# Optimization experiments

Measured on AMD Instinct MI355X. Metric: run time of the kernel, lower is better.

Reference implementation:

```python
import jax, jax.numpy as jnp
import numpy as np

B, S, I = 16, 512, 64
D, H, L, F = 512, 8, 6, 2048
MAX_REL = 32
EPS = 1e-5


def setup_inputs() -> dict:
    key = jax.random.key(0)
    ks = jax.random.split(key, 16)
    sc = 0.02
    inp = {
        "x": jax.random.normal(ks[0], (B, S, I), dtype=jnp.float32),
        "in_W": jax.random.normal(ks[1], (I, D), dtype=jnp.float32) * sc,
        "in_b": jnp.zeros((D,), jnp.float32),
        "rel_emb": jax.random.normal(ks[2], (2 * MAX_REL + 1, D), dtype=jnp.float32) * sc,
        "qkvo_W": jax.random.normal(ks[3], (L, 4, D, D), dtype=jnp.float32) * sc,
        "qkvo_b": jnp.zeros((L, 4, D), jnp.float32),
        "ln_g": jnp.ones((L, 2, D), jnp.float32),
        "ln_b": jnp.zeros((L, 2, D), jnp.float32),
        "ff_W1": jax.random.normal(ks[4], (L, D, F), dtype=jnp.float32) * sc,
        "ff_b1": jnp.zeros((L, F), jnp.float32),
        "ff_W2": jax.random.normal(ks[5], (L, F, D), dtype=jnp.float32) * sc,
        "ff_b2": jnp.zeros((L, D), jnp.float32),
        "out_W": jax.random.normal(ks[6], (D, 1), dtype=jnp.float32) * sc,
        "out_b": jnp.zeros((1,), jnp.float32),
    }
    return inp


def _layernorm(x, g, b):
    mu = jnp.mean(x, axis=-1, keepdims=True)
    var = jnp.mean((x - mu) ** 2, axis=-1, keepdims=True)
    return (x - mu) * jax.lax.rsqrt(var + EPS) * g + b


def reference(x, in_W, in_b, rel_emb, qkvo_W, qkvo_b, ln_g, ln_b, ff_W1, ff_b1, ff_W2, ff_b2, out_W, out_b):
    b, s, _ = x.shape
    dk = D // H
    h = x @ in_W + in_b  # (B,S,D)
    # relative positional encoding: mean over query axis of gathered embeddings
    pos = jnp.arange(s)
    rel = jnp.clip(pos[:, None] - pos[None, :], -MAX_REL, MAX_REL) + MAX_REL  # (S,S)
    rp = rel_emb[rel]  # (S,S,D)
    h = h + rp.mean(axis=0)[None]  # broadcast over batch

    def layer(h, p):
        Wqkvo, bqkvo, g, bl, W1, b1, W2, b2 = p
        def proj(i):
            return (h @ Wqkvo[i] + bqkvo[i]).reshape(b, s, H, dk).transpose(0, 2, 1, 3)
        q, k, v = proj(0), proj(1), proj(2)  # (B,H,S,dk)
        scores = jnp.einsum("bhqd,bhkd->bhqk", q, k) / jnp.sqrt(jnp.float32(dk))
        attn = jax.nn.softmax(scores, axis=-1)
        ctx = jnp.einsum("bhqk,bhkd->bhqd", attn, v)
        ctx = ctx.transpose(0, 2, 1, 3).reshape(b, s, D)
        ao = ctx @ Wqkvo[3] + bqkvo[3]
        h1 = _layernorm(h + ao, g[0], bl[0])
        ff = jax.nn.relu(h1 @ W1 + b1) @ W2 + b2
        h2 = _layernorm(h1 + ff, g[1], bl[1])
        return h2, None

    h, _ = jax.lax.scan(layer, h, (qkvo_W, qkvo_b, ln_g, ln_b, ff_W1, ff_b1, ff_W2, ff_b2))
    out = h @ out_W + out_b  # (B,S,1)
    return out
```

## Files before the change

### kernel.cpp

```cpp
#include <hip/hip_runtime.h>
#include <math.h>

#define B 16
#define S 512
#define IN 64
#define D 512
#define H 8
#define DK 64
#define L 6
#define F 2048
#define BS (B*S)
#define EPS 1e-5f

typedef short short8 __attribute__((ext_vector_type(8)));
typedef short short4v __attribute__((ext_vector_type(4)));
typedef float floatx4 __attribute__((ext_vector_type(4)));

static __device__ inline short f2bf(float x) {
    unsigned u = __float_as_uint(x);
    unsigned r = (u + 0x7fffu + ((u >> 16) & 1u)) >> 16;
    return (short)r;
}
static __device__ inline float bf2f(short s) {
    return __uint_as_float(((unsigned)(unsigned short)s) << 16);
}

__global__ __launch_bounds__(256) void pe_kernel(const float* __restrict__ rel_emb,
                                                 float* __restrict__ pe) {
    int k = blockIdx.x;
    int d = threadIdx.x;
    float acc0 = 0.f, acc1 = 0.f;
    for (int r = 0; r < 65; ++r) {
        float w;
        if (r == 0)       w = (float)max(0, k - 31);
        else if (r == 64) w = (float)max(0, S - (k + 32));
        else {
            int qpos = k + r - 32;
            w = (qpos >= 0 && qpos < S) ? 1.f : 0.f;
        }
        acc0 += w * rel_emb[r * D + d];
        acc1 += w * rel_emb[r * D + d + 256];
    }
    pe[k * D + d]       = acc0 * (1.f / (float)S);
    pe[k * D + d + 256] = acc1 * (1.f / (float)S);
}

__global__ __launch_bounds__(256) void wtrans_kernel(const float* __restrict__ src,
                                                     short* __restrict__ dst,
                                                     int K, int N) {
    __shared__ float Ls[32][33];
    const int z = blockIdx.z, kb = blockIdx.y, nb = blockIdx.x;
    const int tx = threadIdx.x & 31, ty = threadIdx.x >> 5;
    src += (size_t)z * K * N;
    dst += (size_t)z * K * N;
#pragma unroll
    for (int i = 0; i < 4; ++i)
        Ls[ty + i * 8][tx] = src[(size_t)(kb * 32 + ty + i * 8) * N + nb * 32 + tx];
    __syncthreads();
#pragma unroll
    for (int i = 0; i < 4; ++i) {
        int n = nb * 32 + ty + i * 8;
        dst[(size_t)n * K + kb * 32 + tx] = f2bf(Ls[tx][ty + i * 8]);
    }
}

__global__ __launch_bounds__(256) void cvt_kernel(const float* __restrict__ in,
                                                  short* __restrict__ out) {
    int i = (blockIdx.x * 256 + threadIdx.x) * 4;
    float4 v = *(const float4*)(in + i);
    short4v o;
    o.x = f2bf(v.x); o.y = f2bf(v.y); o.z = f2bf(v.z); o.w = f2bf(v.w);
    *(short4v*)(out + i) = o;
}

__global__ __launch_bounds__(256) void vtrans_kernel(const short* __restrict__ v,
                                                     short* __restrict__ vt) {
    __shared__ short Ls[64 * 72];
    const int bh = blockIdx.y, jt = blockIdx.x * 64;
    const int t = threadIdx.x;
    const int r = t >> 2, cg = t & 3;
    *(short8*)&Ls[r * 72 + cg * 8] =
        *(const short8*)(v + ((size_t)bh * S + jt + r) * DK + cg * 8);
    *(short8*)&Ls[r * 72 + 32 + cg * 8] =
        *(const short8*)(v + ((size_t)bh * S + jt + r) * DK + 32 + cg * 8);
    __syncthreads();
    const int d = t >> 2, sg = t & 3;
    short tmp[16];
#pragma unroll
    for (int i = 0; i < 16; ++i) tmp[i] = Ls[(sg * 16 + i) * 72 + d];
    short* dst = vt + ((size_t)bh * DK + d) * S + jt + sg * 16;
    *(short8*)(dst)     = *(short8*)&tmp[0];
    *(short8*)(dst + 8) = *(short8*)&tmp[8];
}

#define GLL(SRC, DST) __builtin_amdgcn_global_load_lds( \
    (const __attribute__((address_space(1))) void*)(SRC), \
    (__attribute__((address_space(3))) void*)(DST), 16, 0, 0)

__global__ __launch_bounds__(256) void mfma_gemm(
    const short* __restrict__ A, const short* __restrict__ Bt,
    const float* __restrict__ bias, short* __restrict__ Cb,
    int M, int N, int K, int mode,
    const float* __restrict__ pe, long wz, long bz, long cz)
{
    __shared__ short As[2][128 * 32];
    __shared__ short Bs[2][128 * 32];

    const int z = blockIdx.z;
    const short* Bz = Bt + (size_t)z * wz;
    const float* bb = bias + (size_t)z * bz;

    const int t = threadIdx.x;
    const int w = t >> 6, lane = t & 63;
    const int wm = w >> 1, wn = w & 1;
    const int ln15 = lane & 15, lq = lane >> 4;
    const int bm = blockIdx.y, bn = blockIdx.x;

    const int ml = lane >> 2;
    const int kb = ((lane & 3) - (ml >> 1)) & 3;
    const short* Ag0 = A  + (size_t)(bm * 128 + w * 16 + ml)       * K + kb * 8;
    const short* Ag1 = A  + (size_t)(bm * 128 + (w + 4) * 16 + ml) * K + kb * 8;
    const short* Bg0 = Bz + (size_t)(bn * 128 + w * 16 + ml)       * K + kb * 8;
    const short* Bg1 = Bz + (size_t)(bn * 128 + (w + 4) * 16 + ml) * K + kb * 8;
    const int so0 = w * 512, so1 = (w + 4) * 512;

    floatx4 acc[4][4] = {};
    const int slot = ln15 * 4 + ((lq + (ln15 >> 1)) & 3);

    GLL(Ag0, &As[0][so0]);
    GLL(Ag1, &As[0][so1]);
    GLL(Bg0, &Bs[0][so0]);
    GLL(Bg1, &Bs[0][so1]);

    int buf = 0;
    for (int kt = 0; kt < K; kt += 32) {
        __syncthreads();
        const int ktn = kt + 32;
        if (ktn < K) {
            GLL(Ag0 + ktn, &As[buf ^ 1][so0]);
            GLL(Ag1 + ktn, &As[buf ^ 1][so1]);
            GLL(Bg0 + ktn, &Bs[buf ^ 1][so0]);
            GLL(Bg1 + ktn, &Bs[buf ^ 1][so1]);
        }
        short8 af[4], bf[4];
#pragma unroll
        for (int mt = 0; mt < 4; ++mt) {
            af[mt] = *(const short8*)&As[buf][((wm * 4 + mt) * 64 + slot) * 8];
            bf[mt] = *(const short8*)&Bs[buf][((wn * 4 + mt) * 64 + slot) * 8];
        }
#pragma unroll
        for (int mt = 0; mt < 4; ++mt)
#pragma unroll
            for (int nt = 0; nt < 4; ++nt)
                acc[mt][nt] = __builtin_amdgcn_mfma_f32_16x16x32_bf16(
                    af[mt], bf[nt], acc[mt][nt], 0, 0, 0);
        buf ^= 1;
    }

    short* Cbz = Cb + (size_t)z * cz;
#pragma unroll
    for (int mt = 0; mt < 4; ++mt) {
#pragma unroll
        for (int nt = 0; nt < 4; ++nt) {
            const int col = bn * 128 + wn * 64 + nt * 16 + ln15;
            const int row0 = bm * 128 + wm * 64 + mt * 16 + lq * 4;
            const float bc = bb[col];
#pragma unroll
            for (int reg = 0; reg < 4; ++reg) {
                const int r = row0 + reg;
                float v = acc[mt][nt][reg] + bc;
                if (mode == 1) v = fmaxf(v, 0.f);
                else if (mode == 2) v += pe[(size_t)(r & (S - 1)) * D + col];
                if (mode == 3) {
                    const int bi = r >> 9, si = r & (S - 1);
                    const int hh = col >> 6, dd = col & 63;
                    Cbz[(((size_t)(bi * H + hh) * S + si) * DK + dd)] = f2bf(v);
                } else {
                    Cb[(size_t)r * N + col] = f2bf(v);
                }
            }
        }
    }
}

__global__ __launch_bounds__(256) void attn_mfma(
    const short* __restrict__ qg, const short* __restrict__ kg,
    const short* __restrict__ vtg, short* __restrict__ ctx)
{
    __shared__ short Ks[64 * 72];
    __shared__ short Vs[64 * 72];
    __shared__ short Ps[4][16 * 72];

    const int t = threadIdx.x;
    const int w = t >> 6, lane = t & 63;
    const int ln15 = lane & 15, lq = lane >> 4;
    const int bh = blockIdx.y, bi = bh >> 3, hh = bh & 7;
    const int qbase = blockIdx.x * 64 + w * 16;

    short8 qf0, qf1;
    {
        const short* qrow = qg + ((size_t)bh * S + qbase + ln15) * DK;
        qf0 = *(const short8*)(qrow + lq * 8);
        qf1 = *(const short8*)(qrow + 32 + lq * 8);
    }
    floatx4 o[4] = {};
    float mrow[4] = {-1e30f, -1e30f, -1e30f, -1e30f};
    float lrow[4] = {};

    const int sr = t >> 2, scg = t & 3;
    const short* kbase = kg  + (size_t)bh * S * DK;
    const short* vtb   = vtg + (size_t)bh * DK * S;

    for (int jt = 0; jt < S; jt += 64) {
        __syncthreads();
        *(short8*)&Ks[sr * 72 + scg * 8] =
            *(const short8*)(kbase + (size_t)(jt + sr) * DK + scg * 8);
        *(short8*)&Ks[sr * 72 + 32 + scg * 8] =
            *(const short8*)(kbase + (size_t)(jt + sr) * DK + 32 + scg * 8);
        *(short8*)&Vs[sr * 72 + scg * 8] =
            *(const short8*)(vtb + (size_t)sr * S + jt + scg * 8);
        *(short8*)&Vs[sr * 72 + 32 + scg * 8] =
            *(const short8*)(vtb + (size_t)sr * S + jt + 32 + scg * 8);
        __syncthreads();

        floatx4 sc[4];
#pragma unroll
        for (int nt = 0; nt < 4; ++nt) {
            floatx4 s4 = {};
            short8 kf0 = *(const short8*)&Ks[(nt * 16 + ln15) * 72 + lq * 8];
            short8 kf1 = *(const short8*)&Ks[(nt * 16 + ln15) * 72 + 32 + lq * 8];
            s4 = __builtin_amdgcn_mfma_f32_16x16x32_bf16(qf0, kf0, s4, 0, 0, 0);
            s4 = __builtin_amdgcn_mfma_f32_16x16x32_bf16(qf1, kf1, s4, 0, 0, 0);
#pragma unroll
            for (int r = 0; r < 4; ++r) s4[r] *= 0.125f;
            sc[nt] = s4;
        }

        float rmax[4];
#pragma unroll
        for (int r = 0; r < 4; ++r)
            rmax[r] = fmaxf(fmaxf(sc[0][r], sc[1][r]), fmaxf(sc[2][r], sc[3][r]));
#pragma unroll
        for (int off = 1; off < 16; off <<= 1)
#pragma unroll
            for (int r = 0; r < 4; ++r)
                rmax[r] = fmaxf(rmax[r], __shfl_xor(rmax[r], off));

        float mnew[4], alpha[4], psum[4];
#pragma unroll
        for (int r = 0; r < 4; ++r) {
            mnew[r]  = fmaxf(mrow[r], rmax[r]);
            alpha[r] = __expf(mrow[r] - mnew[r]);
            psum[r]  = 0.f;
        }
#pragma unroll
        for (int nt = 0; nt < 4; ++nt)
#pragma unroll
            for (int r = 0; r < 4; ++r) {
                float p = __expf(sc[nt][r] - mnew[r]);
                psum[r] += p;
                Ps[w][(lq * 4 + r) * 72 + nt * 16 + ln15] = f2bf(p);
            }
#pragma unroll
        for (int off = 1; off < 16; off <<= 1)
#pragma unroll
            for (int r = 0; r < 4; ++r)
                psum[r] += __shfl_xor(psum[r], off);
#pragma unroll
        for (int r = 0; r < 4; ++r) {
            lrow[r] = lrow[r] * alpha[r] + psum[r];
            mrow[r] = mnew[r];
        }
#pragma unroll
        for (int dv = 0; dv < 4; ++dv)
#pragma unroll
            for (int r = 0; r < 4; ++r)
                o[dv][r] *= alpha[r];

        short8 pf0 = *(const short8*)&Ps[w][ln15 * 72 + lq * 8];
        short8 pf1 = *(const short8*)&Ps[w][ln15 * 72 + 32 + lq * 8];
#pragma unroll
        for (int dv = 0; dv < 4; ++dv) {
            short8 vf0 = *(const short8*)&Vs[(dv * 16 + ln15) * 72 + lq * 8];
            short8 vf1 = *(const short8*)&Vs[(dv * 16 + ln15) * 72 + 32 + lq * 8];
            o[dv] = __builtin_amdgcn_mfma_f32_16x16x32_bf16(pf0, vf0, o[dv], 0, 0, 0);
            o[dv] = __builtin_amdgcn_mfma_f32_16x16x32_bf16(pf1, vf1, o[dv], 0, 0, 0);
        }
    }

    float inv[4];
#pragma unroll
    for (int r = 0; r < 4; ++r) inv[r] = 1.f / lrow[r];
#pragma unroll
    for (int dv = 0; dv < 4; ++dv)
#pragma unroll
        for (int r = 0; r < 4; ++r) {
            const int s = qbase + lq * 4 + r;
            const int col = hh * DK + dv * 16 + ln15;
            ctx[((size_t)bi * S + s) * D + col] = f2bf(o[dv][r] * inv[r]);
        }
}

__global__ __launch_bounds__(128) void ln_kernel(
    const short* __restrict__ a, const short* __restrict__ bres,
    const float* __restrict__ g, const float* __restrict__ beta,
    short* __restrict__ outb)
{
    const int row = blockIdx.x;
    const int t = threadIdx.x;
    const short4v xa = *(const short4v*)(a    + (size_t)row * D + t * 4);
    const short4v xb = *(const short4v*)(bres + (size_t)row * D + t * 4);
    float x0 = bf2f(xa.x) + bf2f(xb.x), x1 = bf2f(xa.y) + bf2f(xb.y);
    float x2 = bf2f(xa.z) + bf2f(xb.z), x3 = bf2f(xa.w) + bf2f(xb.w);
    float s  = x0 + x1 + x2 + x3;
    float s2 = x0 * x0 + x1 * x1 + x2 * x2 + x3 * x3;
#pragma unroll
    for (int o = 32; o > 0; o >>= 1) {
        s  += __shfl_down(s, o);
        s2 += __shfl_down(s2, o);
    }
    __shared__ float red[2][2];
    const int wave = t >> 6;
    if ((t & 63) == 0) { red[wave][0] = s; red[wave][1] = s2; }
    __syncthreads();
    s  = red[0][0] + red[1][0];
    s2 = red[0][1] + red[1][1];
    const float mu  = s * (1.f / (float)D);
    const float var = s2 * (1.f / (float)D) - mu * mu;
    const float r   = rsqrtf(var + EPS);
    const float4 gg = *(const float4*)(g    + t * 4);
    const float4 bb = *(const float4*)(beta + t * 4);
    short4v ob;
    ob.x = f2bf((x0 - mu) * r * gg.x + bb.x);
    ob.y = f2bf((x1 - mu) * r * gg.y + bb.y);
    ob.z = f2bf((x2 - mu) * r * gg.z + bb.z);
    ob.w = f2bf((x3 - mu) * r * gg.w + bb.w);
    *(short4v*)(outb + (size_t)row * D + t * 4) = ob;
}

__global__ __launch_bounds__(256) void out_kernel(
    const short* __restrict__ h, const float* __restrict__ ow,
    const float* __restrict__ ob, float* __restrict__ out)
{
    const int wave = threadIdx.x >> 6;
    const int lane = threadIdx.x & 63;
    const int row  = blockIdx.x * 4 + wave;
    const short* hp = h + (size_t)row * D;
    float s = 0.f;
#pragma unroll
    for (int u = 0; u < 8; ++u) {
        int d = lane + u * 64;
        s += bf2f(hp[d]) * ow[d];
    }
#pragma unroll
    for (int o = 32; o > 0; o >>= 1) s += __shfl_down(s, o);
    if (lane == 0) out[row] = s + ob[0];
}

extern "C" void kernel_launch(void* const* d_in, const int* in_sizes, int n_in,
                              void* d_out, int out_size, void* d_ws, size_t ws_size,
                              hipStream_t stream) {
    const float* x       = (const float*)d_in[0];
    const float* in_W    = (const float*)d_in[1];
    const float* in_b    = (const float*)d_in[2];
    const float* rel_emb = (const float*)d_in[3];
    const float* qkvo_W  = (const float*)d_in[4];
    const float* qkvo_b  = (const float*)d_in[5];
    const float* ln_g    = (const float*)d_in[6];
    const float* ln_bb   = (const float*)d_in[7];
    const float* ff_W1   = (const float*)d_in[8];
    const float* ff_b1   = (const float*)d_in[9];
    const float* ff_W2   = (const float*)d_in[10];
    const float* ff_b2   = (const float*)d_in[11];
    const float* out_W   = (const float*)d_in[12];
    const float* out_b   = (const float*)d_in[13];
    float* out = (float*)d_out;

    const size_t HSZ = (size_t)BS * D;
    float* pe     = (float*)d_ws;
    short* h_bf   = (short*)(pe + (size_t)S * D);
    short* h1_bf  = h_bf  + HSZ;
    short* tmp_bf = h1_bf + HSZ;
    short* qkv_bf = tmp_bf + HSZ;
    short* xb     = qkv_bf + 4 * HSZ;
    short* wt_qkvo = xb + (size_t)BS * IN;
    short* wt_ff1  = wt_qkvo + (size_t)L * 4 * D * D;
    short* wt_ff2  = wt_ff1  + (size_t)L * D * F;
    short* wt_in   = wt_ff2  + (size_t)L * F * D;

    const size_t CZ = (size_t)B * H * S * DK;
    short* qb = qkv_bf;
    short* kb = qkv_bf + CZ;
    short* vb = qkv_bf + 2 * CZ;
    short* vt = qkv_bf + 3 * CZ;
    short* ctx_bf = vb;
    short* ff1_bf = qkv_bf;

    dim3 blk(256);

    pe_kernel<<<dim3(S), blk, 0, stream>>>(rel_emb, pe);
    cvt_kernel<<<dim3(BS * IN / 1024), blk, 0, stream>>>(x, xb);
    wtrans_kernel<<<dim3(D / 32, IN / 32, 1), blk, 0, stream>>>(in_W, wt_in, IN, D);
    wtrans_kernel<<<dim3(D / 32, D / 32, 4 * L), blk, 0, stream>>>(qkvo_W, wt_qkvo, D, D);
    wtrans_kernel<<<dim3(F / 32, D / 32, L), blk, 0, stream>>>(ff_W1, wt_ff1, D, F);
    wtrans_kernel<<<dim3(D / 32, F / 32, L), blk, 0, stream>>>(ff_W2, wt_ff2, F, D);

    mfma_gemm<<<dim3(D / 128, BS / 128, 1), blk, 0, stream>>>(
        xb, wt_in, in_b, h_bf, BS, D, IN, 2, pe, 0, 0, 0);

    for (int l = 0; l < L; ++l) {
        const float* bl = qkvo_b + (size_t)l * 4 * D;
        mfma_gemm<<<dim3(D / 128, BS / 128, 3), blk, 0, stream>>>(
            h_bf, wt_qkvo + (size_t)l * 4 * D * D, bl, qkv_bf, BS, D, D, 3,
            nullptr, (long)D * D, (long)D, (long)CZ);
        vtrans_kernel<<<dim3(S / 64, B * H), blk, 0, stream>>>(vb, vt);
        attn_mfma<<<dim3(S / 64, B * H), blk, 0, stream>>>(qb, kb, vt, ctx_bf);
        mfma_gemm<<<dim3(D / 128, BS / 128, 1), blk, 0, stream>>>(
            ctx_bf, wt_qkvo + (size_t)(l * 4 + 3) * D * D, bl + 3 * D, tmp_bf,
            BS, D, D, 0, nullptr, 0, 0, 0);
        ln_kernel<<<dim3(BS), dim3(128), 0, stream>>>(
            h_bf, tmp_bf, ln_g + (size_t)l * 2 * D, ln_bb + (size_t)l * 2 * D, h1_bf);
        mfma_gemm<<<dim3(F / 128, BS / 128, 1), blk, 0, stream>>>(
            h1_bf, wt_ff1 + (size_t)l * D * F, ff_b1 + (size_t)l * F, ff1_bf,
            BS, F, D, 1, nullptr, 0, 0, 0);
        mfma_gemm<<<dim3(D / 128, BS / 128, 1), blk, 0, stream>>>(
            ff1_bf, wt_ff2 + (size_t)l * F * D, ff_b2 + (size_t)l * D, tmp_bf,
            BS, D, F, 0, nullptr, 0, 0, 0);
        ln_kernel<<<dim3(BS), dim3(128), 0, stream>>>(
            h1_bf, tmp_bf, ln_g + (size_t)l * 2 * D + D, ln_bb + (size_t)l * 2 * D + D,
            h_bf);
    }

    out_kernel<<<dim3(BS / 4), blk, 0, stream>>>(h_bf, out_W, out_b, out);
}
```

Measured before the change: 1.271 ms.

## Split-K the Wo and FF2 GEMMs and reduce partials inside layernorm

The output-projection and second FFN GEMMs now split K in two via blockIdx.z, writing fp32 partial results to two buffers. The residual layernorm kernel sums both partials, the bias and the residual before normalising. This doubles the block count for these N=512 GEMMs so more compute units are busy. In exchange it adds fp32 partial traffic to and from memory, and the workspace layout changes.

```diff
diff --git a/kernel.cpp b/kernel.cpp
--- a/kernel.cpp
+++ b/kernel.cpp
@@ -100,15 +100,15 @@
 __global__ __launch_bounds__(256) void mfma_gemm(
     const short* __restrict__ A, const short* __restrict__ Bt,
     const float* __restrict__ bias, short* __restrict__ Cb,
-    int M, int N, int K, int mode,
-    const float* __restrict__ pe, long wz, long bz, long cz)
+    float* __restrict__ Cf, int M, int N, int K, int lda, int ldb, int mode,
+    const float* __restrict__ pe, long az, long wz, long bz, long cz)
 {
     __shared__ short As[2][128 * 32];
     __shared__ short Bs[2][128 * 32];
 
     const int z = blockIdx.z;
+    const short* Az = A  + (size_t)z * az;
     const short* Bz = Bt + (size_t)z * wz;
-    const float* bb = bias + (size_t)z * bz;
 
     const int t = threadIdx.x;
     const int w = t >> 6, lane = t & 63;
@@ -118,10 +118,10 @@
 
     const int ml = lane >> 2;
     const int kb = ((lane & 3) - (ml >> 1)) & 3;
-    const short* Ag0 = A  + (size_t)(bm * 128 + w * 16 + ml)       * K + kb * 8;
-    const short* Ag1 = A  + (size_t)(bm * 128 + (w + 4) * 16 + ml) * K + kb * 8;
-    const short* Bg0 = Bz + (size_t)(bn * 128 + w * 16 + ml)       * K + kb * 8;
-    const short* Bg1 = Bz + (size_t)(bn * 128 + (w + 4) * 16 + ml) * K + kb * 8;
+    const short* Ag0 = Az + (size_t)(bm * 128 + w * 16 + ml)       * lda + kb * 8;
+    const short* Ag1 = Az + (size_t)(bm * 128 + (w + 4) * 16 + ml) * lda + kb * 8;
+    const short* Bg0 = Bz + (size_t)(bn * 128 + w * 16 + ml)       * ldb + kb * 8;
+    const short* Bg1 = Bz + (size_t)(bn * 128 + (w + 4) * 16 + ml) * ldb + kb * 8;
     const int so0 = w * 512, so1 = (w + 4) * 512;
 
     floatx4 acc[4][4] = {};
@@ -158,24 +158,28 @@
     }
 
     short* Cbz = Cb + (size_t)z * cz;
+    float* Cfz = Cf + (size_t)z * cz;
+    const float* bb = bias + (size_t)z * bz;
 #pragma unroll
     for (int mt = 0; mt < 4; ++mt) {
 #pragma unroll
         for (int nt = 0; nt < 4; ++nt) {
             const int col = bn * 128 + wn * 64 + nt * 16 + ln15;
             const int row0 = bm * 128 + wm * 64 + mt * 16 + lq * 4;
-            const float bc = bb[col];
+            const float bc = (mode == 4) ? 0.f : bb[col];
 #pragma unroll
             for (int reg = 0; reg < 4; ++reg) {
                 const int r = row0 + reg;
                 float v = acc[mt][nt][reg] + bc;
-                if (mode == 1) v = fmaxf(v, 0.f);
-                else if (mode == 2) v += pe[(size_t)(r & (S - 1)) * D + col];
-                if (mode == 3) {
+                if (mode == 4) {
+                    Cfz[(size_t)r * N + col] = v;
+                } else if (mode == 3) {
                     const int bi = r >> 9, si = r & (S - 1);
                     const int hh = col >> 6, dd = col & 63;
                     Cbz[(((size_t)(bi * H + hh) * S + si) * DK + dd)] = f2bf(v);
                 } else {
+                    if (mode == 1) v = fmaxf(v, 0.f);
+                    else if (mode == 2) v += pe[(size_t)(r & (S - 1)) * D + col];
                     Cb[(size_t)r * N + col] = f2bf(v);
                 }
             }
@@ -301,17 +305,23 @@
         }
 }
 
-__global__ __launch_bounds__(128) void ln_kernel(
-    const short* __restrict__ a, const short* __restrict__ bres,
+__global__ __launch_bounds__(128) void ln_res_kernel(
+    const short* __restrict__ a, const float* __restrict__ p0,
+    const float* __restrict__ p1, const float* __restrict__ eb,
     const float* __restrict__ g, const float* __restrict__ beta,
     short* __restrict__ outb)
 {
     const int row = blockIdx.x;
     const int t = threadIdx.x;
-    const short4v xa = *(const short4v*)(a    + (size_t)row * D + t * 4);
-    const short4v xb = *(const short4v*)(bres + (size_t)row * D + t * 4);
-    float x0 = bf2f(xa.x) + bf2f(xb.x), x1 = bf2f(xa.y) + bf2f(xb.y);
-    float x2 = bf2f(xa.z) + bf2f(xb.z), x3 = bf2f(xa.w) + bf2f(xb.w);
+    const size_t off = (size_t)row * D + t * 4;
+    const short4v xa = *(const short4v*)(a + off);
+    const float4 q0 = *(const float4*)(p0 + off);
+    const float4 q1 = *(const float4*)(p1 + off);
+    const float4 bb2 = *(const float4*)(eb + t * 4);
+    float x0 = bf2f(xa.x) + q0.x + q1.x + bb2.x;
+    float x1 = bf2f(xa.y) + q0.y + q1.y + bb2.y;
+    float x2 = bf2f(xa.z) + q0.z + q1.z + bb2.z;
+    float x3 = bf2f(xa.w) + q0.w + q1.w + bb2.w;
     float s  = x0 + x1 + x2 + x3;
     float s2 = x0 * x0 + x1 * x1 + x2 * x2 + x3 * x3;
 #pragma unroll
@@ -335,7 +345,7 @@
     ob.y = f2bf((x1 - mu) * r * gg.y + bb.y);
     ob.z = f2bf((x2 - mu) * r * gg.z + bb.z);
     ob.w = f2bf((x3 - mu) * r * gg.w + bb.w);
-    *(short4v*)(outb + (size_t)row * D + t * 4) = ob;
+    *(short4v*)(outb + off) = ob;
 }
 
 __global__ __launch_bounds__(256) void out_kernel(
@@ -378,10 +388,11 @@
 
     const size_t HSZ = (size_t)BS * D;
     float* pe     = (float*)d_ws;
-    short* h_bf   = (short*)(pe + (size_t)S * D);
+    float* part0  = pe + (size_t)S * D;
+    float* part1  = part0 + HSZ;
+    short* h_bf   = (short*)(part1 + HSZ);
     short* h1_bf  = h_bf  + HSZ;
-    short* tmp_bf = h1_bf + HSZ;
-    short* qkv_bf = tmp_bf + HSZ;
+    short* qkv_bf = h1_bf + HSZ;
     short* xb     = qkv_bf + 4 * HSZ;
     short* wt_qkvo = xb + (size_t)BS * IN;
     short* wt_ff1  = wt_qkvo + (size_t)L * 4 * D * D;
@@ -406,29 +417,30 @@
     wtrans_kernel<<<dim3(D / 32, F / 32, L), blk, 0, stream>>>(ff_W2, wt_ff2, F, D);
 
     mfma_gemm<<<dim3(D / 128, BS / 128, 1), blk, 0, stream>>>(
-        xb, wt_in, in_b, h_bf, BS, D, IN, 2, pe, 0, 0, 0);
+        xb, wt_in, in_b, h_bf, nullptr, BS, D, IN, IN, IN, 2, pe, 0, 0, 0, 0);
 
     for (int l = 0; l < L; ++l) {
         const float* bl = qkvo_b + (size_t)l * 4 * D;
         mfma_gemm<<<dim3(D / 128, BS / 128, 3), blk, 0, stream>>>(
-            h_bf, wt_qkvo + (size_t)l * 4 * D * D, bl, qkv_bf, BS, D, D, 3,
-            nullptr, (long)D * D, (long)D, (long)CZ);
+            h_bf, wt_qkvo + (size_t)l * 4 * D * D, bl, qkv_bf, nullptr,
+            BS, D, D, D, D, 3, nullptr, 0, (long)D * D, (long)D, (long)CZ);
         vtrans_kernel<<<dim3(S / 64, B * H), blk, 0, stream>>>(vb, vt);
         attn_mfma<<<dim3(S / 64, B * H), blk, 0, stream>>>(qb, kb, vt, ctx_bf);
-        mfma_gemm<<<dim3(D / 128, BS / 128, 1), blk, 0, stream>>>(
-            ctx_bf, wt_qkvo + (size_t)(l * 4 + 3) * D * D, bl + 3 * D, tmp_bf,
-            BS, D, D, 0, nullptr, 0, 0, 0);
-        ln_kernel<<<dim3(BS), dim3(128), 0, stream>>>(
-            h_bf, tmp_bf, ln_g + (size_t)l * 2 * D, ln_bb + (size_t)l * 2 * D, h1_bf);
+        mfma_gemm<<<dim3(D / 128, BS / 128, 2), blk, 0, stream>>>(
+            ctx_bf, wt_qkvo + (size_t)(l * 4 + 3) * D * D, nullptr, nullptr, part0,
+            BS, D, 256, D, D, 4, nullptr, 256, 256, 0, (long)HSZ);
+        ln_res_kernel<<<dim3(BS), dim3(128), 0, stream>>>(
+            h_bf, part0, part1, bl + 3 * D,
+            ln_g + (size_t)l * 2 * D, ln_bb + (size_t)l * 2 * D, h1_bf);
         mfma_gemm<<<dim3(F / 128, BS / 128, 1), blk, 0, stream>>>(
-            h1_bf, wt_ff1 + (size_t)l * D * F, ff_b1 + (size_t)l * F, ff1_bf,
-            BS, F, D, 1, nullptr, 0, 0, 0);
-        mfma_gemm<<<dim3(D / 128, BS / 128, 1), blk, 0, stream>>>(
-            ff1_bf, wt_ff2 + (size_t)l * F * D, ff_b2 + (size_t)l * D, tmp_bf,
-            BS, D, F, 0, nullptr, 0, 0, 0);
-        ln_kernel<<<dim3(BS), dim3(128), 0, stream>>>(
-            h1_bf, tmp_bf, ln_g + (size_t)l * 2 * D + D, ln_bb + (size_t)l * 2 * D + D,
-            h_bf);
+            h1_bf, wt_ff1 + (size_t)l * D * F, ff_b1 + (size_t)l * F, ff1_bf, nullptr,
+            BS, F, D, D, D, 1, nullptr, 0, 0, 0, 0);
+        mfma_gemm<<<dim3(D / 128, BS / 128, 2), blk, 0, stream>>>(
+            ff1_bf, wt_ff2 + (size_t)l * F * D, nullptr, nullptr, part0,
+            BS, D, 1024, F, F, 4, nullptr, 1024, 1024, 0, (long)HSZ);
+        ln_res_kernel<<<dim3(BS), dim3(128), 0, stream>>>(
+            h1_bf, part0, part1, ff_b2 + (size_t)l * D,
+            ln_g + (size_t)l * 2 * D + D, ln_bb + (size_t)l * 2 * D + D, h_bf);
     }
 
     out_kernel<<<dim3(BS / 4), blk, 0, stream>>>(h_bf, out_W, out_b, out);
```

Measured after the change: 1.231 ms. 1.03x faster.
